# Performance work log

Measured on AMD Instinct MI355X. Metric: run time of the kernel, lower is better.

Reference implementation:

```python
import jax, jax.numpy as jnp
import numpy as np

B, D, G, OUT = 8, 65536, 1024, 4096  # batch, in_features, n_groups, out_features


def setup_inputs() -> dict:
    key = jax.random.key(0)
    kx, kw = jax.random.split(key)
    x = jax.random.normal(kx, (B, D), dtype=jnp.float32)
    # flat weight table replacing the NVMe file: group g occupies [g*D, (g+1)*D)
    weights = jax.random.normal(kw, (G * D,), dtype=jnp.float32)
    # sorted, contiguous, non-overlapping value ranges covering randn support
    bounds = jnp.linspace(-6.0, 6.0, G + 1, dtype=jnp.float32)
    min_vals = bounds[:-1]
    max_vals = bounds[1:]
    start_pos = jnp.zeros((G,), dtype=jnp.int32)
    offsets = jnp.arange(G, dtype=jnp.int32) * D  # element offsets into weights
    sizes = jnp.full((G,), D, dtype=jnp.int32)
    out_mask = jnp.ones((OUT,), dtype=bool)  # every out_idx has metadata
    return {"x": x, "weights": weights, "min_vals": min_vals, "max_vals": max_vals,
            "start_pos": start_pos, "offsets": offsets, "sizes": sizes, "out_mask": out_mask}


def reference(x, weights, min_vals, max_vals, start_pos, offsets, sizes, out_mask):
    b, d = x.shape
    # original: x[0, in_idx] if batch==1 else x[:, in_idx].mean()
    v = x[0] if b == 1 else x.mean(axis=0)  # [D]
    # vectorized binary search over sorted [min, max] ranges
    g = jnp.searchsorted(min_vals, v, side='right') - 1  # candidate group per input
    gc = jnp.clip(g, 0, min_vals.shape[0] - 1)
    in_range = (g >= 0) & (v >= min_vals[gc]) & (v <= max_vals[gc])
    pos = jnp.arange(d, dtype=jnp.int32) - start_pos[gc]  # pos_in_group
    valid = in_range & (pos >= 0) & (pos < sizes[gc])
    widx = jnp.clip(offsets[gc] + pos, 0, weights.shape[0] - 1)
    w = jnp.where(valid, weights[widx], jnp.float32(0.0))  # gather from table
    s = jnp.sum(v * w)  # scalar MAC accumulated into output[0, out_idx]
    # group lookup ignores output_idx, so every masked out column gets the same sum
    out = jnp.zeros((b, out_mask.shape[0]), dtype=x.dtype)
    out = out.at[0].set(jnp.where(out_mask, s, jnp.float32(0.0)))
    return out
```

## Files before the change

kernel.cpp:

```cpp
#include <hip/hip_runtime.h>

#define BB 8
#define DD 65536
#define GG 1024
#define OUTN 4096

__global__ __launch_bounds__(256) void ril_partials(
    const float* __restrict__ x,
    const float* __restrict__ weights,
    const float* __restrict__ min_vals,
    const float* __restrict__ max_vals,
    const int* __restrict__ start_pos,
    const int* __restrict__ offsets,
    const int* __restrict__ sizes,
    float* __restrict__ partials,
    int wlen)
{
    __shared__ float s_min[GG];
    __shared__ float s_max[GG];
    __shared__ int   s_start[GG];
    __shared__ int   s_off[GG];
    __shared__ int   s_size[GG];

    const int t = threadIdx.x;
    for (int i = t; i < GG; i += 256) {
        s_min[i]   = min_vals[i];
        s_max[i]   = max_vals[i];
        s_start[i] = start_pos[i];
        s_off[i]   = offsets[i];
        s_size[i]  = sizes[i];
    }
    __syncthreads();

    const int d = blockIdx.x * 256 + t;

    float v = 0.0f;
#pragma unroll
    for (int b = 0; b < BB; ++b) v += x[b * DD + d];
    v *= (1.0f / BB);

    int lo = 0, hi = GG;
#pragma unroll
    while (lo < hi) {
        int mid = (lo + hi) >> 1;
        if (s_min[mid] <= v) lo = mid + 1; else hi = mid;
    }
    const int g  = lo - 1;
    const int gc = min(max(g, 0), GG - 1);

    const bool in_range = (g >= 0) && (v >= s_min[gc]) && (v <= s_max[gc]);
    const int  pos      = d - s_start[gc];
    const bool valid    = in_range && (pos >= 0) && (pos < s_size[gc]);

    int widx = s_off[gc] + pos;
    widx = min(max(widx, 0), wlen - 1);
    const float w = valid ? weights[widx] : 0.0f;

    float p = v * w;

#pragma unroll
    for (int off = 32; off > 0; off >>= 1) p += __shfl_down(p, off);

    __shared__ float s_wsum[4];
    if ((t & 63) == 0) s_wsum[t >> 6] = p;
    __syncthreads();
    if (t == 0) partials[blockIdx.x] = (s_wsum[0] + s_wsum[1]) + (s_wsum[2] + s_wsum[3]);
}

__global__ __launch_bounds__(256) void ril_finalize(
    const float* __restrict__ partials,
    const int* __restrict__ out_mask,
    float* __restrict__ out)
{
    const int t = threadIdx.x;

    float p = partials[t];
#pragma unroll
    for (int off = 32; off > 0; off >>= 1) p += __shfl_down(p, off);

    __shared__ float s_wsum[4];
    __shared__ float s_total;
    if ((t & 63) == 0) s_wsum[t >> 6] = p;
    __syncthreads();
    if (t == 0) s_total = (s_wsum[0] + s_wsum[1]) + (s_wsum[2] + s_wsum[3]);
    __syncthreads();
    const float s = s_total;

    const int i = blockIdx.x * 256 + t;
    float val = 0.0f;
    if (i < OUTN && out_mask[i] != 0) val = s;
    out[i] = val;
}

extern "C" void kernel_launch(void* const* d_in, const int* in_sizes, int n_in,
                              void* d_out, int out_size, void* d_ws, size_t ws_size,
                              hipStream_t stream) {
    const float* x        = (const float*)d_in[0];
    const float* weights  = (const float*)d_in[1];
    const float* min_vals = (const float*)d_in[2];
    const float* max_vals = (const float*)d_in[3];
    const int*   start_p  = (const int*)d_in[4];
    const int*   offsets  = (const int*)d_in[5];
    const int*   sizes    = (const int*)d_in[6];
    const int*   out_mask = (const int*)d_in[7];
    float* out = (float*)d_out;
    float* partials = (float*)d_ws;

    const int wlen = in_sizes[1];

    ril_partials<<<DD / 256, 256, 0, stream>>>(
        x, weights, min_vals, max_vals, start_p, offsets, sizes, partials, wlen);

    ril_finalize<<<(BB * OUTN) / 256, 256, 0, stream>>>(partials, out_mask, out);
}
```

Before: 11.08 us.

## Replace shared-memory binary search with interpolated group guess and linear correction

Drops the per-block staging of all five 1024-entry metadata tables into LDS and the binary search over them. Each thread instead guesses its group by linear interpolation between the first and last min values, then corrects it by stepping through global min_vals. Blocks shrink to a single 64-lane wave so no LDS reduction or barrier is needed, and the finalize kernel folds the four times larger partial array and writes its output with 128-bit vector stores. The interpolation guess only stays cheap when the group bounds are close to uniform; badly skewed bounds would make the correction loop long.

```diff
diff --git a/kernel.cpp b/kernel.cpp
--- a/kernel.cpp
+++ b/kernel.cpp
@@ -5,7 +5,7 @@
 #define GG 1024
 #define OUTN 4096
 
-__global__ __launch_bounds__(256) void ril_partials(
+__global__ __launch_bounds__(64) void ril_partials(
     const float* __restrict__ x,
     const float* __restrict__ weights,
     const float* __restrict__ min_vals,
@@ -16,43 +16,44 @@
     float* __restrict__ partials,
     int wlen)
 {
-    __shared__ float s_min[GG];
-    __shared__ float s_max[GG];
-    __shared__ int   s_start[GG];
-    __shared__ int   s_off[GG];
-    __shared__ int   s_size[GG];
+    const int t = threadIdx.x;
+    const int d = blockIdx.x * 64 + t;
 
-    const int t = threadIdx.x;
-    for (int i = t; i < GG; i += 256) {
-        s_min[i]   = min_vals[i];
-        s_max[i]   = max_vals[i];
-        s_start[i] = start_pos[i];
-        s_off[i]   = offsets[i];
-        s_size[i]  = sizes[i];
-    }
-    __syncthreads();
+    float x0 = x[0 * DD + d];
+    float x1 = x[1 * DD + d];
+    float x2 = x[2 * DD + d];
+    float x3 = x[3 * DD + d];
+    float x4 = x[4 * DD + d];
+    float x5 = x[5 * DD + d];
+    float x6 = x[6 * DD + d];
+    float x7 = x[7 * DD + d];
 
-    const int d = blockIdx.x * 256 + t;
+    const float m0    = min_vals[0];
+    const float mlast = min_vals[GG - 1];
 
-    float v = 0.0f;
-#pragma unroll
-    for (int b = 0; b < BB; ++b) v += x[b * DD + d];
-    v *= (1.0f / BB);
+    const float v = (((x0 + x1) + (x2 + x3)) + ((x4 + x5) + (x6 + x7))) * 0.125f;
 
-    int lo = 0, hi = GG;
-#pragma unroll
-    while (lo < hi) {
-        int mid = (lo + hi) >> 1;
-        if (s_min[mid] <= v) lo = mid + 1; else hi = mid;
-    }
-    const int g  = lo - 1;
+    float inv = (mlast > m0) ? (float)(GG - 1) / (mlast - m0) : 0.0f;
+    float gf = (v - m0) * inv;
+    gf = fminf(fmaxf(gf, -1.0f), (float)(GG - 1));
+    int gi = (int)floorf(gf);
+    while (gi + 1 < GG && min_vals[gi + 1] <= v) ++gi;
+    while (gi >= 0 && min_vals[gi] > v) --gi;
+
+    const int g  = gi;
     const int gc = min(max(g, 0), GG - 1);
 
-    const bool in_range = (g >= 0) && (v >= s_min[gc]) && (v <= s_max[gc]);
-    const int  pos      = d - s_start[gc];
-    const bool valid    = in_range && (pos >= 0) && (pos < s_size[gc]);
+    const float mn = min_vals[gc];
+    const float mx = max_vals[gc];
+    const int   sp = start_pos[gc];
+    const int   of = offsets[gc];
+    const int   sz = sizes[gc];
 
-    int widx = s_off[gc] + pos;
+    const bool in_range = (g >= 0) && (v >= mn) && (v <= mx);
+    const int  pos      = d - sp;
+    const bool valid    = in_range && (pos >= 0) && (pos < sz);
+
+    int widx = of + pos;
     widx = min(max(widx, 0), wlen - 1);
     const float w = valid ? weights[widx] : 0.0f;
 
@@ -61,10 +62,7 @@
 #pragma unroll
     for (int off = 32; off > 0; off >>= 1) p += __shfl_down(p, off);
 
-    __shared__ float s_wsum[4];
-    if ((t & 63) == 0) s_wsum[t >> 6] = p;
-    __syncthreads();
-    if (t == 0) partials[blockIdx.x] = (s_wsum[0] + s_wsum[1]) + (s_wsum[2] + s_wsum[3]);
+    if (t == 0) partials[blockIdx.x] = p;
 }
 
 __global__ __launch_bounds__(256) void ril_finalize(
@@ -74,7 +72,7 @@
 {
     const int t = threadIdx.x;
 
-    float p = partials[t];
+    float p = (partials[t] + partials[t + 256]) + (partials[t + 512] + partials[t + 768]);
 #pragma unroll
     for (int off = 32; off > 0; off >>= 1) p += __shfl_down(p, off);
 
@@ -86,10 +84,16 @@
     __syncthreads();
     const float s = s_total;
 
-    const int i = blockIdx.x * 256 + t;
-    float val = 0.0f;
-    if (i < OUTN && out_mask[i] != 0) val = s;
-    out[i] = val;
+    const int q = (blockIdx.x * 256 + t) * 4;
+    float4 val = {0.0f, 0.0f, 0.0f, 0.0f};
+    if (q < OUTN) {
+        const int4 m = *reinterpret_cast<const int4*>(&out_mask[q]);
+        val.x = m.x ? s : 0.0f;
+        val.y = m.y ? s : 0.0f;
+        val.z = m.z ? s : 0.0f;
+        val.w = m.w ? s : 0.0f;
+    }
+    *reinterpret_cast<float4*>(&out[q]) = val;
 }
 
 extern "C" void kernel_launch(void* const* d_in, const int* in_sizes, int n_in,
@@ -108,8 +112,8 @@
 
     const int wlen = in_sizes[1];
 
-    ril_partials<<<DD / 256, 256, 0, stream>>>(
+    ril_partials<<<DD / 64, 64, 0, stream>>>(
         x, weights, min_vals, max_vals, start_p, offsets, sizes, partials, wlen);
 
-    ril_finalize<<<(BB * OUTN) / 256, 256, 0, stream>>>(partials, out_mask, out);
+    ril_finalize<<<(BB * OUTN) / (256 * 4), 256, 0, stream>>>(partials, out_mask, out);
 }
```

Measured after the change: 11.10 us. About the same (+0.2%).
